# Performance work log

Measured on AMD Instinct MI355X. Metric: run time of the kernel, lower is better.

The kernel has to match this reference:

```python
import jax, jax.numpy as jnp
import numpy as np

IN_FEATURES = 8192
OUT_FEATURES = 28672
RANK = 32
GROUP = 64          # int4 quantization group size along in_features
M_TOKENS = 16       # decode-style batch of tokens
PAD = 128           # kernel requires in dim padded to multiple of 128


def setup_inputs() -> dict:
    key = jax.random.key(0)
    k0, k1, k2, k3, k4, k5 = jax.random.split(key, 6)
    x = jax.random.normal(k0, (M_TOKENS, IN_FEATURES), dtype=jnp.float16)
    # int4 codes in [-8, 7], stored unpacked as int32
    qweight = jax.random.randint(k1, (OUT_FEATURES, IN_FEATURES), 0, 16, dtype=jnp.int32) - 8
    # positive per-(out_channel, group) dequant scales, realistic small magnitude
    wscales = (jax.random.uniform(k2, (OUT_FEATURES, IN_FEATURES // GROUP), dtype=jnp.float16)
               * jnp.float16(0.02) + jnp.float16(0.001))
    # low-rank SVD correction branch (LoRA-style)
    lora_down = jax.random.normal(k3, (RANK, IN_FEATURES), dtype=jnp.float16) * jnp.float16(0.02)
    lora_up = jax.random.normal(k4, (OUT_FEATURES, RANK), dtype=jnp.float16) * jnp.float16(0.02)
    bias = jax.random.normal(k5, (OUT_FEATURES,), dtype=jnp.float16)
    return {"x": x, "qweight": qweight, "wscales": wscales,
            "lora_down": lora_down, "lora_up": lora_up, "bias": bias}


def reference(x, qweight, wscales, lora_down, lora_up, bias):
    # Pad input features to a multiple of 128 (as the CUDA kernel requires).
    in_pad = ((IN_FEATURES + PAD - 1) // PAD) * PAD
    if x.shape[-1] != in_pad:
        x = jnp.pad(x, ((0, 0), (0, in_pad - x.shape[-1])))
    xk = x[:, :IN_FEATURES]  # padded columns hit zero weight columns; equivalent

    # Dequantize: W[o, k] = q[o, k] * scale[o, k // GROUP]   -> [out, in] fp16
    w = qweight.astype(jnp.float16) * jnp.repeat(wscales, GROUP, axis=1)

    # Quantized GEMM + low-rank correction + bias (all fused in the real kernel)
    y = jnp.matmul(xk, w.T)                                   # [M, out]
    y = y + jnp.matmul(jnp.matmul(xk, lora_down.T), lora_up.T)  # rank-RANK branch
    y = y + bias
    return y[:, :OUT_FEATURES]
```

## Files before the change

kernel.cpp:

```cpp
#include <hip/hip_runtime.h>
#include <hip/hip_bf16.h>

#define IN_F 8192
#define OUT_F 28672
#define RANK 32
#define NGROUPS 128
#define M_TOK 16
#define TCHUNK 16
#define TCK (IN_F / TCHUNK)
#define KSPLIT 4
#define KW (IN_F / KSPLIT)

typedef __bf16 bf16x8 __attribute__((ext_vector_type(8)));
typedef float  f32x4  __attribute__((ext_vector_type(4)));
typedef int    i32x4  __attribute__((ext_vector_type(4)));

__global__ __launch_bounds__(256) void svdq_xcast(
    const float* __restrict__ x, __bf16* __restrict__ xb) {
  const int i = blockIdx.x * 256 + threadIdx.x;
  f32x4 a = reinterpret_cast<const f32x4*>(x)[i * 2];
  f32x4 b = reinterpret_cast<const f32x4*>(x)[i * 2 + 1];
  bf16x8 v;
#pragma unroll
  for (int j = 0; j < 4; ++j) { v[j] = (__bf16)a[j]; v[j + 4] = (__bf16)b[j]; }
  reinterpret_cast<bf16x8*>(xb)[i] = v;
}

__global__ __launch_bounds__(512) void svdq_tpart(
    const float* __restrict__ x, const float* __restrict__ ld,
    float* __restrict__ part) {
  const int c = blockIdx.x;
  const int i = threadIdx.x;
  const int m = i >> 5, r = i & 31;
  const f32x4* xp = reinterpret_cast<const f32x4*>(x  + (size_t)m * IN_F + c * TCK);
  const f32x4* lp = reinterpret_cast<const f32x4*>(ld + (size_t)r * IN_F + c * TCK);
  float s = 0.f;
#pragma unroll 8
  for (int j = 0; j < TCK / 4; ++j) {
    f32x4 a = xp[j], b = lp[j];
    s += a[0]*b[0] + a[1]*b[1] + a[2]*b[2] + a[3]*b[3];
  }
  part[(size_t)c * (M_TOK * RANK) + i] = s;
}

__global__ __launch_bounds__(256) void svdq_main(
    const __bf16* __restrict__ xb, const int* __restrict__ qw,
    const float* __restrict__ wsc, const float* __restrict__ lu,
    const float* __restrict__ bias, const float* __restrict__ part,
    float* __restrict__ out) {
  const int w    = threadIdx.x >> 6;
  const int lane = threadIdx.x & 63;
  const int col  = lane & 15;
  const int hi   = lane >> 4;
  const int o    = blockIdx.x * 16 + col;

  const int*    qrow = qw  + (size_t)o * IN_F + w * KW + hi * 8;
  const __bf16* xrow = xb  + (size_t)col * IN_F + w * KW + hi * 8;
  const float*  srow = wsc + (size_t)o * NGROUPS + w * (KW / 64);

  f32x4 acc = {0.f, 0.f, 0.f, 0.f};

#pragma unroll 1
  for (int g8 = 0; g8 < KW / 512; ++g8) {
    f32x4 sA = *reinterpret_cast<const f32x4*>(srow + g8 * 8);
    f32x4 sB = *reinterpret_cast<const f32x4*>(srow + g8 * 8 + 4);
#pragma unroll
    for (int kk = 0; kk < 16; ++kk) {
      const int k0 = g8 * 512 + kk * 32;
      i32x4 q0 = *reinterpret_cast<const i32x4*>(qrow + k0);
      i32x4 q1 = *reinterpret_cast<const i32x4*>(qrow + k0 + 4);
      bf16x8 a = *reinterpret_cast<const bf16x8*>(xrow + k0);
      const int   sidx = kk >> 1;
      const float s = (sidx < 4) ? sA[sidx] : sB[sidx - 4];
      bf16x8 b;
#pragma unroll
      for (int j = 0; j < 4; ++j) {
        b[j]     = (__bf16)((float)q0[j] * s);
        b[j + 4] = (__bf16)((float)q1[j] * s);
      }
      acc = __builtin_amdgcn_mfma_f32_16x16x32_bf16(a, b, acc, 0, 0, 0);
    }
  }

  __shared__ float red[KSPLIT][64][4];
#pragma unroll
  for (int r = 0; r < 4; ++r) red[w][lane][r] = acc[r];
  __syncthreads();
  if (threadIdx.x >= 64) return;

  f32x4 tot = {0.f, 0.f, 0.f, 0.f};
#pragma unroll
  for (int ww = 0; ww < KSPLIT; ++ww) {
    f32x4 v = *reinterpret_cast<const f32x4*>(&red[ww][lane][0]);
    tot += v;
  }

  f32x4 t0 = {0.f,0.f,0.f,0.f}, t1 = {0.f,0.f,0.f,0.f};
#pragma unroll
  for (int c = 0; c < TCHUNK; ++c) {
    const f32x4* pc = reinterpret_cast<const f32x4*>(
        part + (size_t)c * (M_TOK * RANK) + col * RANK + hi * 8);
    t0 += pc[0];
    t1 += pc[1];
  }
  f32x4 u0 = *reinterpret_cast<const f32x4*>(lu + (size_t)o * RANK + hi * 8);
  f32x4 u1 = *reinterpret_cast<const f32x4*>(lu + (size_t)o * RANK + hi * 8 + 4);
  bf16x8 ta, lb;
#pragma unroll
  for (int j = 0; j < 4; ++j) {
    ta[j]     = (__bf16)t0[j];
    ta[j + 4] = (__bf16)t1[j];
    lb[j]     = (__bf16)u0[j];
    lb[j + 4] = (__bf16)u1[j];
  }
  f32x4 lacc = {0.f, 0.f, 0.f, 0.f};
  lacc = __builtin_amdgcn_mfma_f32_16x16x32_bf16(ta, lb, lacc, 0, 0, 0);

  const float bv = bias[o];
#pragma unroll
  for (int reg = 0; reg < 4; ++reg) {
    const int m = hi * 4 + reg;
    out[(size_t)m * OUT_F + o] = tot[reg] + lacc[reg] + bv;
  }
}

extern "C" void kernel_launch(void* const* d_in, const int* in_sizes, int n_in,
                              void* d_out, int out_size, void* d_ws, size_t ws_size,
                              hipStream_t stream) {
  const float* x    = (const float*)d_in[0];
  const int*   qw   = (const int*)d_in[1];
  const float* wsc  = (const float*)d_in[2];
  const float* ld   = (const float*)d_in[3];
  const float* lu   = (const float*)d_in[4];
  const float* bias = (const float*)d_in[5];
  float*       out  = (float*)d_out;

  float*  part = (float*)d_ws;
  __bf16* xbf  = (__bf16*)((char*)d_ws + 64 * 1024);

  svdq_xcast<<<M_TOK * IN_F / (256 * 8), 256, 0, stream>>>(x, xbf);
  svdq_tpart<<<TCHUNK, 512, 0, stream>>>(x, ld, part);
  svdq_main<<<OUT_F / 16, 256, 0, stream>>>(xbf, qw, wsc, lu, bias, part, out);
}
```

Measured before the change: 242.1 us.

## Compute four output tiles per block to reuse activation loads across MFMAs

Each block now covers 64 output channels instead of 16, with each wave issuing four dequant+MFMA sequences per k-step that share one activation fragment load. The cross-wave reduction is restructured so all four waves take part in the epilogue, each finishing one 16-column tile. The aim is to cut redundant activation reads and give each wave more independent memory and MFMA work in flight. The costs are more registers and 4x fewer blocks (448 versus 1792), which could lower occupancy and the number of loads in flight for this bandwidth-bound int32 weight stream.

```diff
diff --git a/kernel.cpp b/kernel.cpp
--- a/kernel.cpp
+++ b/kernel.cpp
@@ -10,6 +10,7 @@
 #define TCK (IN_F / TCHUNK)
 #define KSPLIT 4
 #define KW (IN_F / KSPLIT)
+#define NT 4
 
 typedef __bf16 bf16x8 __attribute__((ext_vector_type(8)));
 typedef float  f32x4  __attribute__((ext_vector_type(4)));
@@ -48,52 +49,81 @@
     const float* __restrict__ wsc, const float* __restrict__ lu,
     const float* __restrict__ bias, const float* __restrict__ part,
     float* __restrict__ out) {
-  const int w    = threadIdx.x >> 6;
-  const int lane = threadIdx.x & 63;
-  const int col  = lane & 15;
-  const int hi   = lane >> 4;
-  const int o    = blockIdx.x * 16 + col;
+  const int w     = threadIdx.x >> 6;
+  const int lane  = threadIdx.x & 63;
+  const int col   = lane & 15;
+  const int hi    = lane >> 4;
+  const int obase = blockIdx.x * (16 * NT);
 
-  const int*    qrow = qw  + (size_t)o * IN_F + w * KW + hi * 8;
-  const __bf16* xrow = xb  + (size_t)col * IN_F + w * KW + hi * 8;
-  const float*  srow = wsc + (size_t)o * NGROUPS + w * (KW / 64);
+  const __bf16* xrow = xb + (size_t)col * IN_F + w * KW + hi * 8;
+  const int*   qrow0 = qw + (size_t)(obase +  0 + col) * IN_F + w * KW + hi * 8;
+  const int*   qrow1 = qw + (size_t)(obase + 16 + col) * IN_F + w * KW + hi * 8;
+  const int*   qrow2 = qw + (size_t)(obase + 32 + col) * IN_F + w * KW + hi * 8;
+  const int*   qrow3 = qw + (size_t)(obase + 48 + col) * IN_F + w * KW + hi * 8;
+  const float* srow0 = wsc + (size_t)(obase +  0 + col) * NGROUPS + w * (KW / 64);
+  const float* srow1 = wsc + (size_t)(obase + 16 + col) * NGROUPS + w * (KW / 64);
+  const float* srow2 = wsc + (size_t)(obase + 32 + col) * NGROUPS + w * (KW / 64);
+  const float* srow3 = wsc + (size_t)(obase + 48 + col) * NGROUPS + w * (KW / 64);
 
-  f32x4 acc = {0.f, 0.f, 0.f, 0.f};
+  f32x4 acc0 = {0.f,0.f,0.f,0.f}, acc1 = {0.f,0.f,0.f,0.f};
+  f32x4 acc2 = {0.f,0.f,0.f,0.f}, acc3 = {0.f,0.f,0.f,0.f};
 
 #pragma unroll 1
   for (int g8 = 0; g8 < KW / 512; ++g8) {
-    f32x4 sA = *reinterpret_cast<const f32x4*>(srow + g8 * 8);
-    f32x4 sB = *reinterpret_cast<const f32x4*>(srow + g8 * 8 + 4);
+    f32x4 sA0 = *reinterpret_cast<const f32x4*>(srow0 + g8 * 8);
+    f32x4 sB0 = *reinterpret_cast<const f32x4*>(srow0 + g8 * 8 + 4);
+    f32x4 sA1 = *reinterpret_cast<const f32x4*>(srow1 + g8 * 8);
+    f32x4 sB1 = *reinterpret_cast<const f32x4*>(srow1 + g8 * 8 + 4);
+    f32x4 sA2 = *reinterpret_cast<const f32x4*>(srow2 + g8 * 8);
+    f32x4 sB2 = *reinterpret_cast<const f32x4*>(srow2 + g8 * 8 + 4);
+    f32x4 sA3 = *reinterpret_cast<const f32x4*>(srow3 + g8 * 8);
+    f32x4 sB3 = *reinterpret_cast<const f32x4*>(srow3 + g8 * 8 + 4);
 #pragma unroll
     for (int kk = 0; kk < 16; ++kk) {
-      const int k0 = g8 * 512 + kk * 32;
-      i32x4 q0 = *reinterpret_cast<const i32x4*>(qrow + k0);
-      i32x4 q1 = *reinterpret_cast<const i32x4*>(qrow + k0 + 4);
+      const int k0   = g8 * 512 + kk * 32;
+      const int sidx = kk >> 1;
       bf16x8 a = *reinterpret_cast<const bf16x8*>(xrow + k0);
-      const int   sidx = kk >> 1;
-      const float s = (sidx < 4) ? sA[sidx] : sB[sidx - 4];
-      bf16x8 b;
-#pragma unroll
-      for (int j = 0; j < 4; ++j) {
-        b[j]     = (__bf16)((float)q0[j] * s);
-        b[j + 4] = (__bf16)((float)q1[j] * s);
+
+#define DEQ_MFMA(QR, SA, SB, ACC)                                            \
+      {                                                                      \
+        i32x4 q0 = *reinterpret_cast<const i32x4*>(QR + k0);                 \
+        i32x4 q1 = *reinterpret_cast<const i32x4*>(QR + k0 + 4);             \
+        const float s = (sidx < 4) ? SA[sidx] : SB[sidx - 4];                \
+        bf16x8 b;                                                            \
+        _Pragma("unroll")                                                    \
+        for (int j = 0; j < 4; ++j) {                                        \
+          b[j]     = (__bf16)((float)q0[j] * s);                             \
+          b[j + 4] = (__bf16)((float)q1[j] * s);                             \
+        }                                                                    \
+        ACC = __builtin_amdgcn_mfma_f32_16x16x32_bf16(a, b, ACC, 0, 0, 0);   \
       }
-      acc = __builtin_amdgcn_mfma_f32_16x16x32_bf16(a, b, acc, 0, 0, 0);
+
+      DEQ_MFMA(qrow0, sA0, sB0, acc0)
+      DEQ_MFMA(qrow1, sA1, sB1, acc1)
+      DEQ_MFMA(qrow2, sA2, sB2, acc2)
+      DEQ_MFMA(qrow3, sA3, sB3, acc3)
+#undef DEQ_MFMA
     }
   }
 
-  __shared__ float red[KSPLIT][64][4];
+  __shared__ float red[KSPLIT][64][NT][4];
 #pragma unroll
-  for (int r = 0; r < 4; ++r) red[w][lane][r] = acc[r];
+  for (int r = 0; r < 4; ++r) {
+    red[w][lane][0][r] = acc0[r];
+    red[w][lane][1][r] = acc1[r];
+    red[w][lane][2][r] = acc2[r];
+    red[w][lane][3][r] = acc3[r];
+  }
   __syncthreads();
-  if (threadIdx.x >= 64) return;
 
   f32x4 tot = {0.f, 0.f, 0.f, 0.f};
 #pragma unroll
   for (int ww = 0; ww < KSPLIT; ++ww) {
-    f32x4 v = *reinterpret_cast<const f32x4*>(&red[ww][lane][0]);
+    f32x4 v = *reinterpret_cast<const f32x4*>(&red[ww][lane][w][0]);
     tot += v;
   }
+
+  const int o = obase + w * 16 + col;
 
   f32x4 t0 = {0.f,0.f,0.f,0.f}, t1 = {0.f,0.f,0.f,0.f};
 #pragma unroll
@@ -140,5 +170,5 @@
 
   svdq_xcast<<<M_TOK * IN_F / (256 * 8), 256, 0, stream>>>(x, xbf);
   svdq_tpart<<<TCHUNK, 512, 0, stream>>>(x, ld, part);
-  svdq_main<<<OUT_F / 16, 256, 0, stream>>>(xbf, qw, wsc, lu, bias, part, out);
+  svdq_main<<<OUT_F / (16 * NT), 256, 0, stream>>>(xbf, qw, wsc, lu, bias, part, out);
 }
```

Measured after the change: 255.6 us. +5.6%, slower.

## Double-buffer int4 weight stream through LDS with async global_load_lds prefetch

Applied to the files above, without the earlier changes.

The main GEMM loop now stages each 64-wide K step of the unpacked int32 weights into a per-wave double-buffered LDS region using global_load_lds, and prefetches the next step's activations and scale while computing the current one. Manual vmcnt waits and scheduling barriers keep exactly one step of loads in flight, so memory latency overlaps the dequantize and MFMA work. This adds 32 KB of LDS per block, which may reduce occupancy, and relies on hand-counted vmcnt values being correct.

```diff
diff --git a/kernel.cpp b/kernel.cpp
--- a/kernel.cpp
+++ b/kernel.cpp
@@ -10,10 +10,14 @@
 #define TCK (IN_F / TCHUNK)
 #define KSPLIT 4
 #define KW (IN_F / KSPLIT)
+#define NSTEP (KW / 64)
 
 typedef __bf16 bf16x8 __attribute__((ext_vector_type(8)));
 typedef float  f32x4  __attribute__((ext_vector_type(4)));
 typedef int    i32x4  __attribute__((ext_vector_type(4)));
+
+#define GLOBAL_AS __attribute__((address_space(1)))
+#define LDS_AS    __attribute__((address_space(3)))
 
 __global__ __launch_bounds__(256) void svdq_xcast(
     const float* __restrict__ x, __bf16* __restrict__ xb) {
@@ -56,31 +60,66 @@
 
   const int*    qrow = qw  + (size_t)o * IN_F + w * KW + hi * 8;
   const __bf16* xrow = xb  + (size_t)col * IN_F + w * KW + hi * 8;
-  const float*  srow = wsc + (size_t)o * NGROUPS + w * (KW / 64);
+  const float*  srow = wsc + (size_t)o * NGROUPS + w * NSTEP;
+
+  __shared__ int qbuf[KSPLIT][2][1024];
+  int* mybuf = &qbuf[w][0][0];
+
+#define STAGE(T, B) {                                                         \
+    const int* _s = qrow + (T) * 64;                                          \
+    int* _d = mybuf + (B) * 1024;                                             \
+    __builtin_amdgcn_global_load_lds((const GLOBAL_AS int*)(_s),              \
+                                     (LDS_AS int*)(_d),       16, 0, 0);      \
+    __builtin_amdgcn_global_load_lds((const GLOBAL_AS int*)(_s + 4),          \
+                                     (LDS_AS int*)(_d + 256), 16, 0, 0);      \
+    __builtin_amdgcn_global_load_lds((const GLOBAL_AS int*)(_s + 32),         \
+                                     (LDS_AS int*)(_d + 512), 16, 0, 0);      \
+    __builtin_amdgcn_global_load_lds((const GLOBAL_AS int*)(_s + 36),         \
+                                     (LDS_AS int*)(_d + 768), 16, 0, 0);      \
+  }
 
   f32x4 acc = {0.f, 0.f, 0.f, 0.f};
 
+#define COMPUTE(B, A0, A1, S) {                                               \
+    const int* _b = mybuf + (B) * 1024 + lane * 4;                            \
+    i32x4 q0 = *reinterpret_cast<const i32x4*>(_b);                           \
+    i32x4 q1 = *reinterpret_cast<const i32x4*>(_b + 256);                     \
+    i32x4 q2 = *reinterpret_cast<const i32x4*>(_b + 512);                     \
+    i32x4 q3 = *reinterpret_cast<const i32x4*>(_b + 768);                     \
+    bf16x8 b0, b1;                                                            \
+    _Pragma("unroll")                                                         \
+    for (int j = 0; j < 4; ++j) {                                             \
+      b0[j]     = (__bf16)((float)q0[j] * (S));                               \
+      b0[j + 4] = (__bf16)((float)q1[j] * (S));                               \
+      b1[j]     = (__bf16)((float)q2[j] * (S));                               \
+      b1[j + 4] = (__bf16)((float)q3[j] * (S));                               \
+    }                                                                         \
+    acc = __builtin_amdgcn_mfma_f32_16x16x32_bf16((A0), b0, acc, 0, 0, 0);    \
+    acc = __builtin_amdgcn_mfma_f32_16x16x32_bf16((A1), b1, acc, 0, 0, 0);    \
+  }
+
+  STAGE(0, 0)
+  bf16x8 a0 = *reinterpret_cast<const bf16x8*>(xrow);
+  bf16x8 a1 = *reinterpret_cast<const bf16x8*>(xrow + 32);
+  float  s  = srow[0];
+
 #pragma unroll 1
-  for (int g8 = 0; g8 < KW / 512; ++g8) {
-    f32x4 sA = *reinterpret_cast<const f32x4*>(srow + g8 * 8);
-    f32x4 sB = *reinterpret_cast<const f32x4*>(srow + g8 * 8 + 4);
-#pragma unroll
-    for (int kk = 0; kk < 16; ++kk) {
-      const int k0 = g8 * 512 + kk * 32;
-      i32x4 q0 = *reinterpret_cast<const i32x4*>(qrow + k0);
-      i32x4 q1 = *reinterpret_cast<const i32x4*>(qrow + k0 + 4);
-      bf16x8 a = *reinterpret_cast<const bf16x8*>(xrow + k0);
-      const int   sidx = kk >> 1;
-      const float s = (sidx < 4) ? sA[sidx] : sB[sidx - 4];
-      bf16x8 b;
-#pragma unroll
-      for (int j = 0; j < 4; ++j) {
-        b[j]     = (__bf16)((float)q0[j] * s);
-        b[j + 4] = (__bf16)((float)q1[j] * s);
-      }
-      acc = __builtin_amdgcn_mfma_f32_16x16x32_bf16(a, b, acc, 0, 0, 0);
-    }
+  for (int t = 0; t < NSTEP - 1; ++t) {
+    bf16x8 a0n = *reinterpret_cast<const bf16x8*>(xrow + (t + 1) * 64);
+    bf16x8 a1n = *reinterpret_cast<const bf16x8*>(xrow + (t + 1) * 64 + 32);
+    float  sn  = srow[t + 1];
+    STAGE(t + 1, (t + 1) & 1)
+    asm volatile("s_waitcnt vmcnt(7)" ::: "memory");
+    __builtin_amdgcn_sched_barrier(0);
+    COMPUTE(t & 1, a0, a1, s)
+    a0 = a0n; a1 = a1n; s = sn;
   }
+  asm volatile("s_waitcnt vmcnt(0)" ::: "memory");
+  __builtin_amdgcn_sched_barrier(0);
+  COMPUTE((NSTEP - 1) & 1, a0, a1, s)
+
+#undef STAGE
+#undef COMPUTE
 
   __shared__ float red[KSPLIT][64][4];
 #pragma unroll
```

After: 269.4 us. 1.11x slower.

## Double-buffer weight tiles via async global-to-LDS loads and fuse prep kernels

Applied to the files above, without the earlier changes.

The main GEMM loop now streams int32 weight tiles into swizzled LDS double buffers with global_load_lds, waits on vmcnt, and prefetches the next x and scale values while computing the current tile. This is meant to hide global memory latency on the dominant weight stream. Separately, the bf16 cast of x is folded into the low-rank partial kernel, saving one launch. The cost is 64KB of LDS per block, which limits occupancy, plus a hand-tuned waitcnt that is fragile if the compiler reorders or adds memory ops.

```diff
diff --git a/kernel.cpp b/kernel.cpp
--- a/kernel.cpp
+++ b/kernel.cpp
@@ -10,27 +10,37 @@
 #define TCK (IN_F / TCHUNK)
 #define KSPLIT 4
 #define KW (IN_F / KSPLIT)
+#define NSTEP (KW / 128)
 
 typedef __bf16 bf16x8 __attribute__((ext_vector_type(8)));
 typedef float  f32x4  __attribute__((ext_vector_type(4)));
 typedef int    i32x4  __attribute__((ext_vector_type(4)));
 
-__global__ __launch_bounds__(256) void svdq_xcast(
-    const float* __restrict__ x, __bf16* __restrict__ xb) {
-  const int i = blockIdx.x * 256 + threadIdx.x;
-  f32x4 a = reinterpret_cast<const f32x4*>(x)[i * 2];
-  f32x4 b = reinterpret_cast<const f32x4*>(x)[i * 2 + 1];
-  bf16x8 v;
-#pragma unroll
-  for (int j = 0; j < 4; ++j) { v[j] = (__bf16)a[j]; v[j + 4] = (__bf16)b[j]; }
-  reinterpret_cast<bf16x8*>(xb)[i] = v;
-}
+#define GLOBAL_AS __attribute__((address_space(1)))
+#define LDS_AS    __attribute__((address_space(3)))
 
-__global__ __launch_bounds__(512) void svdq_tpart(
+__global__ __launch_bounds__(512) void svdq_prep(
     const float* __restrict__ x, const float* __restrict__ ld,
-    float* __restrict__ part) {
+    float* __restrict__ part, __bf16* __restrict__ xb) {
   const int c = blockIdx.x;
   const int i = threadIdx.x;
+
+  {
+    const int base = c * 8192 + i * 16;
+    f32x4 f0 = *reinterpret_cast<const f32x4*>(x + base);
+    f32x4 f1 = *reinterpret_cast<const f32x4*>(x + base + 4);
+    f32x4 f2 = *reinterpret_cast<const f32x4*>(x + base + 8);
+    f32x4 f3 = *reinterpret_cast<const f32x4*>(x + base + 12);
+    bf16x8 v0, v1;
+#pragma unroll
+    for (int j = 0; j < 4; ++j) {
+      v0[j] = (__bf16)f0[j]; v0[j + 4] = (__bf16)f1[j];
+      v1[j] = (__bf16)f2[j]; v1[j + 4] = (__bf16)f3[j];
+    }
+    *reinterpret_cast<bf16x8*>(xb + base)     = v0;
+    *reinterpret_cast<bf16x8*>(xb + base + 8) = v1;
+  }
+
   const int m = i >> 5, r = i & 31;
   const f32x4* xp = reinterpret_cast<const f32x4*>(x  + (size_t)m * IN_F + c * TCK);
   const f32x4* lp = reinterpret_cast<const f32x4*>(ld + (size_t)r * IN_F + c * TCK);
@@ -48,52 +58,98 @@
     const float* __restrict__ wsc, const float* __restrict__ lu,
     const float* __restrict__ bias, const float* __restrict__ part,
     float* __restrict__ out) {
-  const int w    = threadIdx.x >> 6;
-  const int lane = threadIdx.x & 63;
-  const int col  = lane & 15;
-  const int hi   = lane >> 4;
-  const int o    = blockIdx.x * 16 + col;
+  const int w     = threadIdx.x >> 6;
+  const int lane  = threadIdx.x & 63;
+  const int col   = lane & 15;
+  const int hi    = lane >> 4;
+  const int l32   = lane & 31;
+  const int rhalf = lane >> 5;
+  const int obase = blockIdx.x * 16;
+  const int o     = obase + col;
 
-  const int*    qrow = qw  + (size_t)o * IN_F + w * KW + hi * 8;
-  const __bf16* xrow = xb  + (size_t)col * IN_F + w * KW + hi * 8;
-  const float*  srow = wsc + (size_t)o * NGROUPS + w * (KW / 64);
+  __shared__ int smem[KSPLIT * 4096];
+  int* mybuf = smem + w * 4096;
+
+  const int*    qbase = qw + (size_t)(obase + rhalf) * IN_F + w * KW;
+  const __bf16* xrow  = xb + (size_t)col * IN_F + w * KW + hi * 8;
+  const float*  srow  = wsc + (size_t)o * NGROUPS + w * (KW / 64);
+
+  int xoff[4];
+#pragma unroll
+  for (int j = 0; j < 4; ++j) xoff[j] = (l32 ^ ((2 * j + rhalf) & 7)) * 4;
+
+#define STAGE(T, B)                                                            \
+  {                                                                            \
+    _Pragma("unroll")                                                          \
+    for (int i = 0; i < 8; ++i) {                                              \
+      const int* _s = qbase + (size_t)(2 * i) * IN_F + (T) * 128 + xoff[i & 3];\
+      __builtin_amdgcn_global_load_lds((const GLOBAL_AS int*)_s,               \
+          (LDS_AS int*)(mybuf + (B) * 2048 + i * 256), 16, 0, 0);              \
+    }                                                                          \
+  }
 
   f32x4 acc = {0.f, 0.f, 0.f, 0.f};
 
-#pragma unroll 1
-  for (int g8 = 0; g8 < KW / 512; ++g8) {
-    f32x4 sA = *reinterpret_cast<const f32x4*>(srow + g8 * 8);
-    f32x4 sB = *reinterpret_cast<const f32x4*>(srow + g8 * 8 + 4);
-#pragma unroll
-    for (int kk = 0; kk < 16; ++kk) {
-      const int k0 = g8 * 512 + kk * 32;
-      i32x4 q0 = *reinterpret_cast<const i32x4*>(qrow + k0);
-      i32x4 q1 = *reinterpret_cast<const i32x4*>(qrow + k0 + 4);
-      bf16x8 a = *reinterpret_cast<const bf16x8*>(xrow + k0);
-      const int   sidx = kk >> 1;
-      const float s = (sidx < 4) ? sA[sidx] : sB[sidx - 4];
-      bf16x8 b;
-#pragma unroll
-      for (int j = 0; j < 4; ++j) {
-        b[j]     = (__bf16)((float)q0[j] * s);
-        b[j + 4] = (__bf16)((float)q1[j] * s);
-      }
-      acc = __builtin_amdgcn_mfma_f32_16x16x32_bf16(a, b, acc, 0, 0, 0);
-    }
+#define COMPUTE(B, A0, A1, A2, A3, SC)                                         \
+  {                                                                            \
+    const int* _base = mybuf + (B) * 2048 + col * 128;                         \
+    const int  _sw   = col & 7;                                                \
+    _Pragma("unroll")                                                          \
+    for (int kk = 0; kk < 4; ++kk) {                                           \
+      const int c0 = kk * 8 + hi * 2;                                          \
+      i32x4 q0 = *reinterpret_cast<const i32x4*>(_base + ((c0 ^ _sw) * 4));    \
+      i32x4 q1 = *reinterpret_cast<const i32x4*>(_base + (((c0 + 1) ^ _sw) * 4));\
+      const float s = (kk < 2) ? (SC).x : (SC).y;                              \
+      bf16x8 b;                                                                \
+      _Pragma("unroll")                                                        \
+      for (int j = 0; j < 4; ++j) {                                            \
+        b[j]     = (__bf16)((float)q0[j] * s);                                 \
+        b[j + 4] = (__bf16)((float)q1[j] * s);                                 \
+      }                                                                        \
+      bf16x8 _a = (kk == 0) ? (A0) : (kk == 1) ? (A1) : (kk == 2) ? (A2) : (A3);\
+      acc = __builtin_amdgcn_mfma_f32_16x16x32_bf16(_a, b, acc, 0, 0, 0);      \
+    }                                                                          \
   }
 
-  __shared__ float red[KSPLIT][64][4];
+  STAGE(0, 0)
+  bf16x8 a0 = *reinterpret_cast<const bf16x8*>(xrow);
+  bf16x8 a1 = *reinterpret_cast<const bf16x8*>(xrow + 32);
+  bf16x8 a2 = *reinterpret_cast<const bf16x8*>(xrow + 64);
+  bf16x8 a3 = *reinterpret_cast<const bf16x8*>(xrow + 96);
+  float2 sc = *reinterpret_cast<const float2*>(srow);
+
+#pragma unroll 1
+  for (int t = 0; t < NSTEP - 1; ++t) {
+    const __bf16* xn = xrow + (t + 1) * 128;
+    bf16x8 n0 = *reinterpret_cast<const bf16x8*>(xn);
+    bf16x8 n1 = *reinterpret_cast<const bf16x8*>(xn + 32);
+    bf16x8 n2 = *reinterpret_cast<const bf16x8*>(xn + 64);
+    bf16x8 n3 = *reinterpret_cast<const bf16x8*>(xn + 96);
+    float2 sn = *reinterpret_cast<const float2*>(srow + (t + 1) * 2);
+    STAGE(t + 1, (t + 1) & 1)
+    asm volatile("s_waitcnt vmcnt(13)" ::: "memory");
+    __builtin_amdgcn_sched_barrier(0);
+    COMPUTE(t & 1, a0, a1, a2, a3, sc)
+    a0 = n0; a1 = n1; a2 = n2; a3 = n3; sc = sn;
+  }
+  asm volatile("s_waitcnt vmcnt(0)" ::: "memory");
+  __builtin_amdgcn_sched_barrier(0);
+  COMPUTE((NSTEP - 1) & 1, a0, a1, a2, a3, sc)
+
+#undef STAGE
+#undef COMPUTE
+
+  __syncthreads();
+  float* red = reinterpret_cast<float*>(smem);
 #pragma unroll
-  for (int r = 0; r < 4; ++r) red[w][lane][r] = acc[r];
+  for (int r = 0; r < 4; ++r) red[(w * 64 + lane) * 4 + r] = acc[r];
   __syncthreads();
   if (threadIdx.x >= 64) return;
 
   f32x4 tot = {0.f, 0.f, 0.f, 0.f};
 #pragma unroll
-  for (int ww = 0; ww < KSPLIT; ++ww) {
-    f32x4 v = *reinterpret_cast<const f32x4*>(&red[ww][lane][0]);
-    tot += v;
-  }
+  for (int ww = 0; ww < KSPLIT; ++ww)
+    tot += *reinterpret_cast<const f32x4*>(red + (ww * 64 + lane) * 4);
 
   f32x4 t0 = {0.f,0.f,0.f,0.f}, t1 = {0.f,0.f,0.f,0.f};
 #pragma unroll
@@ -138,7 +194,6 @@
   float*  part = (float*)d_ws;
   __bf16* xbf  = (__bf16*)((char*)d_ws + 64 * 1024);
 
-  svdq_xcast<<<M_TOK * IN_F / (256 * 8), 256, 0, stream>>>(x, xbf);
-  svdq_tpart<<<TCHUNK, 512, 0, stream>>>(x, ld, part);
+  svdq_prep<<<TCHUNK, 512, 0, stream>>>(x, ld, part, xbf);
   svdq_main<<<OUT_F / 16, 256, 0, stream>>>(xbf, qw, wsc, lu, bias, part, out);
 }
```

Result: faster. 204.4 us (median of 2 runs) (-15.6%).
